# Optimization experiments

Hardware: AMD Instinct MI355X
Metric: run time of the kernel (lower is better)

The kernel has to match this reference:

```python
import jax, jax.numpy as jnp
import numpy as np

T, D, H = 2048, 1024, 16
HS = D // H  # head_size = 64
DFF = 4 * D
LN_EPS = 1e-6


def layernorm(x, scale, bias, eps=LN_EPS):
    mu = jnp.mean(x, axis=-1, keepdims=True)
    var = jnp.mean(jnp.square(x - mu), axis=-1, keepdims=True)
    return (x - mu) * jax.lax.rsqrt(var + eps) * scale + bias


def setup_inputs() -> dict:
    key = jax.random.key(0)
    ks = jax.random.split(key, 12)
    s_in = 1.0 / np.sqrt(D)
    s_ff = 1.0 / np.sqrt(DFF)
    return {
        "x": jax.random.normal(ks[0], (T, D), jnp.float32),
        "Wq": jax.random.normal(ks[1], (H, D, HS), jnp.float32) * s_in,
        "Wk": jax.random.normal(ks[2], (H, D, HS), jnp.float32) * s_in,
        "Wv": jax.random.normal(ks[3], (H, D, HS), jnp.float32) * s_in,
        "Wo": jax.random.normal(ks[4], (D, D), jnp.float32) * s_in,
        "bo": jnp.zeros((D,), jnp.float32),
        "W1": jax.random.normal(ks[5], (D, DFF), jnp.float32) * s_in,
        "b1": jnp.zeros((DFF,), jnp.float32),
        "W2": jax.random.normal(ks[6], (DFF, D), jnp.float32) * s_ff,
        "b2": jnp.zeros((D,), jnp.float32),
        "ln1_scale": jnp.ones((D,), jnp.float32),
        "ln1_bias": jnp.zeros((D,), jnp.float32),
        "ln2_scale": jnp.ones((D,), jnp.float32),
        "ln2_bias": jnp.zeros((D,), jnp.float32),
        "training": 0,
    }


def reference(x, Wq, Wk, Wv, Wo, bo, W1, b1, W2, b2,
              ln1_scale, ln1_bias, ln2_scale, ln2_bias, training):
    # --- pre-LN causal multi-head self-attention ---
    h = layernorm(x, ln1_scale, ln1_bias)
    q = jnp.einsum("td,hdk->htk", h, Wq)  # [H,T,HS]
    k = jnp.einsum("td,hdk->htk", h, Wk)
    v = jnp.einsum("td,hdk->htk", h, Wv)
    scores = jnp.einsum("htk,hsk->hts", q, k) / jnp.sqrt(jnp.float32(HS))
    causal = jnp.tril(jnp.ones((T, T), jnp.float32))
    scores = jnp.where(causal == 0, -jnp.inf, scores)
    wei = jax.nn.softmax(scores, axis=-1)
    av = jnp.einsum("hts,hsk->htk", wei, v)          # [H,T,HS]
    av = av.transpose(1, 0, 2).reshape(T, H * HS)    # concat over heads
    x = x + av @ Wo + bo                              # dropout deterministic -> identity
    # --- pre-LN feed-forward ---
    h2 = layernorm(x, ln2_scale, ln2_bias)
    ff = jax.nn.relu(h2 @ W1 + b1) @ W2 + b2
    x = x + ff
    return x
```

## Files before the change

kernel.cpp:

```cpp
#include <hip/hip_runtime.h>
#include <cstdint>


typedef __bf16 bf16;
typedef __bf16 bf16x4 __attribute__((ext_vector_type(4)));
typedef __bf16 bf16x8 __attribute__((ext_vector_type(8)));
typedef float floatx4 __attribute__((ext_vector_type(4)));

__device__ __forceinline__ void ld_g2l(const bf16* g, bf16* l) {
    __builtin_amdgcn_global_load_lds(
        (const __attribute__((address_space(1))) void*)g,
        (__attribute__((address_space(3))) void*)l, 16, 0, 0);
}

__device__ __forceinline__ void ln_row_body(
    const float* __restrict__ x, const float* __restrict__ sc,
    const float* __restrict__ bi, bf16* __restrict__ out,
    int row, int tid, float* wred)
{
    const float4 v = ((const float4*)(x + (size_t)row * 1024))[tid];
    float s1 = v.x + v.y + v.z + v.w;
    float s2 = v.x * v.x + v.y * v.y + v.z * v.z + v.w * v.w;
#pragma unroll
    for (int mm = 1; mm < 64; mm <<= 1) {
        s1 += __shfl_xor(s1, mm);
        s2 += __shfl_xor(s2, mm);
    }
    const int wave = tid >> 6, lane = tid & 63;
    if (lane == 0) { wred[wave] = s1; wred[4 + wave] = s2; }
    __syncthreads();
    s1 = wred[0] + wred[1] + wred[2] + wred[3];
    s2 = wred[4] + wred[5] + wred[6] + wred[7];
    const float mu = s1 * (1.f / 1024.f);
    const float var = fmaxf(s2 * (1.f / 1024.f) - mu * mu, 0.f);
    const float rr = rsqrtf(var + 1e-6f);
    const float4 scv = ((const float4*)sc)[tid];
    const float4 biv = ((const float4*)bi)[tid];
    bf16x4 ov;
    ov[0] = (bf16)((v.x - mu) * rr * scv.x + biv.x);
    ov[1] = (bf16)((v.y - mu) * rr * scv.y + biv.y);
    ov[2] = (bf16)((v.z - mu) * rr * scv.z + biv.z);
    ov[3] = (bf16)((v.w - mu) * rr * scv.w + biv.w);
    *(bf16x4*)(out + (size_t)row * 1024 + tid * 4) = ov;
}

__global__ __launch_bounds__(256) void prep_kernel(
    const float* __restrict__ Wq, const float* __restrict__ Wk,
    const float* __restrict__ Wv, bf16* __restrict__ Wqkvt,
    const float* __restrict__ Wo, bf16* __restrict__ Wot,
    const float* __restrict__ W1, bf16* __restrict__ W1t,
    const float* __restrict__ W2, bf16* __restrict__ W2t,
    const float* __restrict__ x, const float* __restrict__ ln1s,
    const float* __restrict__ ln1b, bf16* __restrict__ hbuf)
{
    __shared__ float tile[64][65];
    __shared__ float wred[8];
    const int b = blockIdx.x;
    const int tid = threadIdx.x;

    if (b >= 3072) {
        ln_row_body(x, ln1s, ln1b, hbuf, b - 3072, tid, wred);
        return;
    }

    const int tx = tid & 63, ty = tid >> 6;
    const float* src; bf16* dst; int R, C, c0, r0;
    if (b < 768) {
        const int sec = b >> 4, ti = b & 15;
        const int m = sec >> 4, h = sec & 15;
        src = (m == 0 ? Wq : (m == 1 ? Wk : Wv)) + h * 65536;
        dst = Wqkvt + m * 1048576 + h * 65536;
        R = 1024; C = 64; c0 = 0; r0 = ti * 64;
    } else if (b < 1024) {
        const int i = b - 768;
        src = Wo; dst = Wot; R = 1024; C = 1024;
        c0 = (i & 15) * 64; r0 = (i >> 4) * 64;
    } else if (b < 2048) {
        const int i = b - 1024;
        src = W1; dst = W1t; R = 1024; C = 4096;
        c0 = (i & 63) * 64; r0 = (i >> 6) * 64;
    } else {
        const int i = b - 2048;
        src = W2; dst = W2t; R = 4096; C = 1024;
        c0 = (i & 15) * 64; r0 = (i >> 4) * 64;
    }
#pragma unroll
    for (int i = ty; i < 64; i += 4)
        tile[i][tx] = src[(size_t)(r0 + i) * C + c0 + tx];
    __syncthreads();
#pragma unroll
    for (int i = ty; i < 64; i += 4)
        dst[(size_t)(c0 + i) * R + r0 + tx] = (bf16)tile[tx][i];
}

__global__ __launch_bounds__(256) void ln_kernel(
    const float* __restrict__ x, const float* __restrict__ sc,
    const float* __restrict__ bi, bf16* __restrict__ out)
{
    __shared__ float wred[8];
    ln_row_body(x, sc, bi, out, blockIdx.x, threadIdx.x, wred);
}

__global__ __launch_bounds__(256) void transpose_head_kernel(
    const bf16* __restrict__ qkv, bf16* __restrict__ dst, int colOff)
{
    __shared__ bf16 tile[32][33];
    const int tx = threadIdx.x, ty = threadIdx.y;
    const int h = blockIdx.z;
    const int j0 = blockIdx.x * 32, s0 = blockIdx.y * 32;
#pragma unroll
    for (int i = ty; i < 32; i += 8)
        tile[i][tx] = qkv[(size_t)(s0 + i) * 3072 + colOff + h * 64 + j0 + tx];
    __syncthreads();
#pragma unroll
    for (int i = ty; i < 32; i += 8)
        dst[(size_t)h * 64 * 2048 + (size_t)(j0 + i) * 2048 + s0 + tx] = tile[tx][i];
}

__global__ __launch_bounds__(256) void reduce4_kernel(
    const float* __restrict__ p, const float* __restrict__ bias,
    const float* __restrict__ res, float* __restrict__ out)
{
    const int idx = blockIdx.x * 256 + threadIdx.x;
    const int c4 = idx & 255;
    const float4 a0 = ((const float4*)p)[idx];
    const float4 a1 = ((const float4*)(p + 2097152))[idx];
    const float4 a2 = ((const float4*)(p + 4194304))[idx];
    const float4 a3 = ((const float4*)(p + 6291456))[idx];
    const float4 bi = ((const float4*)bias)[c4];
    const float4 r = ((const float4*)res)[idx];
    float4 o;
    o.x = (a0.x + a1.x) + (a2.x + a3.x) + bi.x + r.x;
    o.y = (a0.y + a1.y) + (a2.y + a3.y) + bi.y + r.y;
    o.z = (a0.z + a1.z) + (a2.z + a3.z) + bi.z + r.z;
    o.w = (a0.w + a1.w) + (a2.w + a3.w) + bi.w + r.w;
    ((float4*)out)[idx] = o;
}

template <int MODE, int NG, int MG, int SPLITK>
__global__ __launch_bounds__(256) void gemm128_kernel(
    const bf16* __restrict__ A, const bf16* __restrict__ Bt,
    int N, int K,
    float* __restrict__ outF, bf16* __restrict__ outB,
    const float* __restrict__ bias)
{
    __shared__ __align__(16) bf16 Alds[2][128][64];
    __shared__ __align__(16) bf16 Blds[2][128][64];
    const int tid  = threadIdx.x;
    const int lane = tid & 63;
    const int w    = tid >> 6;
    const int r15  = lane & 15;
    const int quad = lane >> 4;

    const int id    = blockIdx.x + gridDim.x * (blockIdx.y + gridDim.y * blockIdx.z);
    const int xcd   = id & 7;
    const int seq   = id >> 3;
    const int nPerX = gridDim.x / NG;
    const int mPerX = gridDim.y / MG;
    const int nm    = nPerX * mPerX;
    const int z     = seq / nm;
    const int loc   = seq - z * nm;
    const int bn    = ((xcd % NG) * nPerX + (loc % nPerX)) * 128;
    const int bm    = ((xcd / NG) * mPerX + (loc / nPerX)) * 128;

    const int wm = (w >> 1) * 64;
    const int wn = (w & 1) * 64;

    floatx4 acc[4][4];
#pragma unroll
    for (int i = 0; i < 4; ++i)
#pragma unroll
        for (int j = 0; j < 4; ++j) acc[i][j] = (floatx4)(0.f);

    const int KS    = K / SPLITK;
    const int kBase = (SPLITK > 1) ? z * KS : 0;
    const int nIter = KS / 64;

    const int lrow = lane >> 3;
    const int gch  = (lane & 7) ^ lrow;
    const bf16* aptr = A + (size_t)(bm + w * 16 + lrow) * K + kBase + gch * 8;
    const bf16* bptr = Bt + (size_t)(bn + w * 16 + lrow) * K + kBase + gch * 8;

#pragma unroll
    for (int rr = 0; rr < 2; ++rr)
#pragma unroll
        for (int t = 0; t < 2; ++t) {
            ld_g2l(aptr + (size_t)(rr * 64 + t * 8) * K, &Alds[0][rr * 64 + w * 16 + t * 8][0]);
            ld_g2l(bptr + (size_t)(rr * 64 + t * 8) * K, &Blds[0][rr * 64 + w * 16 + t * 8][0]);
        }

    for (int it = 0; it < nIter; ++it) {
        const int buf = it & 1;
        __syncthreads();
        if (it + 1 < nIter) {
            const int k2 = (it + 1) * 64;
#pragma unroll
            for (int rr = 0; rr < 2; ++rr)
#pragma unroll
                for (int t = 0; t < 2; ++t) {
                    ld_g2l(aptr + (size_t)(rr * 64 + t * 8) * K + k2,
                           &Alds[buf ^ 1][rr * 64 + w * 16 + t * 8][0]);
                    ld_g2l(bptr + (size_t)(rr * 64 + t * 8) * K + k2,
                           &Blds[buf ^ 1][rr * 64 + w * 16 + t * 8][0]);
                }
        }
#pragma unroll
        for (int kk = 0; kk < 2; ++kk) {
            const int pc = ((kk * 4 + quad) ^ (r15 & 7)) * 8;
            bf16x8 af[4], bfr[4];
#pragma unroll
            for (int i = 0; i < 4; ++i)
                af[i] = *(const bf16x8*)(&Alds[buf][wm + i * 16 + r15][pc]);
#pragma unroll
            for (int j = 0; j < 4; ++j)
                bfr[j] = *(const bf16x8*)(&Blds[buf][wn + j * 16 + r15][pc]);
#pragma unroll
            for (int i = 0; i < 4; ++i)
#pragma unroll
                for (int j = 0; j < 4; ++j)
                    acc[i][j] = __builtin_amdgcn_mfma_f32_16x16x32_bf16(
                        af[i], bfr[j], acc[i][j], 0, 0, 0);
        }
    }

    const int row0 = bm + wm + quad * 4;
    const int col0 = bn + wn + r15;
    float* po = (MODE == 3) ? outF + (size_t)z * 2048 * 1024 : outF;
#pragma unroll
    for (int i = 0; i < 4; ++i) {
#pragma unroll
        for (int reg = 0; reg < 4; ++reg) {
            const int row = row0 + i * 16 + reg;
#pragma unroll
            for (int j = 0; j < 4; ++j) {
                const int col = col0 + j * 16;
                float v = acc[i][j][reg];
                if (MODE == 0) {
                    outB[(size_t)row * N + col] = (bf16)v;
                } else if (MODE == 2) {
                    v += bias[col];
                    outB[(size_t)row * N + col] = (bf16)fmaxf(v, 0.f);
                } else {
                    po[(size_t)row * N + col] = v;
                }
            }
        }
    }
}

template <int NG, int MG>
__global__ __launch_bounds__(256) void gemm64_kernel(
    const bf16* __restrict__ A, const bf16* __restrict__ Bt,
    int N, int K,
    float* __restrict__ outF, const float* __restrict__ bias,
    const float* __restrict__ res)
{
    __shared__ __align__(16) bf16 Alds[2][64][64];
    __shared__ __align__(16) bf16 Blds[2][64][64];
    const int tid  = threadIdx.x;
    const int lane = tid & 63;
    const int w    = tid >> 6;
    const int r15  = lane & 15;
    const int quad = lane >> 4;

    const int id    = blockIdx.x + gridDim.x * blockIdx.y;
    const int xcd   = id & 7;
    const int seq   = id >> 3;
    const int nPerX = gridDim.x / NG;
    const int mPerX = gridDim.y / MG;
    const int loc   = seq % (nPerX * mPerX);
    const int bn    = ((xcd % NG) * nPerX + (loc % nPerX)) * 64;
    const int bm    = ((xcd / NG) * mPerX + (loc / nPerX)) * 64;

    const int wm = (w >> 1) * 32;
    const int wn = (w & 1) * 32;

    floatx4 acc[2][2];
#pragma unroll
    for (int i = 0; i < 2; ++i)
#pragma unroll
        for (int j = 0; j < 2; ++j) acc[i][j] = (floatx4)(0.f);

    const int nIter = K / 64;
    const int lrow = lane >> 3;
    const int gch  = (lane & 7) ^ lrow;
    const bf16* aptr = A + (size_t)(bm + w * 16 + lrow) * K + gch * 8;
    const bf16* bptr = Bt + (size_t)(bn + w * 16 + lrow) * K + gch * 8;

#pragma unroll
    for (int t = 0; t < 2; ++t) {
        ld_g2l(aptr + (size_t)t * 8 * K, &Alds[0][w * 16 + t * 8][0]);
        ld_g2l(bptr + (size_t)t * 8 * K, &Blds[0][w * 16 + t * 8][0]);
    }

    for (int it = 0; it < nIter; ++it) {
        const int buf = it & 1;
        __syncthreads();
        if (it + 1 < nIter) {
            const int k2 = (it + 1) * 64;
#pragma unroll
            for (int t = 0; t < 2; ++t) {
                ld_g2l(aptr + (size_t)t * 8 * K + k2, &Alds[buf ^ 1][w * 16 + t * 8][0]);
                ld_g2l(bptr + (size_t)t * 8 * K + k2, &Blds[buf ^ 1][w * 16 + t * 8][0]);
            }
        }
#pragma unroll
        for (int kk = 0; kk < 2; ++kk) {
            const int pc = ((kk * 4 + quad) ^ (r15 & 7)) * 8;
            bf16x8 af[2], bfr[2];
#pragma unroll
            for (int i = 0; i < 2; ++i)
                af[i] = *(const bf16x8*)(&Alds[buf][wm + i * 16 + r15][pc]);
#pragma unroll
            for (int j = 0; j < 2; ++j)
                bfr[j] = *(const bf16x8*)(&Blds[buf][wn + j * 16 + r15][pc]);
#pragma unroll
            for (int i = 0; i < 2; ++i)
#pragma unroll
                for (int j = 0; j < 2; ++j)
                    acc[i][j] = __builtin_amdgcn_mfma_f32_16x16x32_bf16(
                        af[i], bfr[j], acc[i][j], 0, 0, 0);
        }
    }

    const int row0 = bm + wm + quad * 4;
    const int col0 = bn + wn + r15;
#pragma unroll
    for (int i = 0; i < 2; ++i)
#pragma unroll
        for (int reg = 0; reg < 4; ++reg) {
            const int row = row0 + i * 16 + reg;
#pragma unroll
            for (int j = 0; j < 2; ++j) {
                const int col = col0 + j * 16;
                outF[(size_t)row * N + col] =
                    acc[i][j][reg] + bias[col] + res[(size_t)row * N + col];
            }
        }
}

__global__ __launch_bounds__(256) void attn_kernel(
    const bf16* __restrict__ qkv, const bf16* __restrict__ vt,
    bf16* __restrict__ Opart, float* __restrict__ Lpart)
{
    __shared__ __align__(16) bf16 Qs[64][64];
    __shared__ __align__(16) bf16 Ks[2][64][64];
    __shared__ __align__(16) bf16 Vs[2][64][64];
    __shared__ __align__(16) bf16 Ps[4][16][72];

    const int tid  = threadIdx.x;
    const int w    = tid >> 6;
    const int lane = tid & 63;
    const int r15  = lane & 15;
    const int quad = lane >> 4;
    const int rl   = lane >> 3;
    const int gsw  = (lane & 7) ^ (rl & 7);

    const int b    = blockIdx.x;
    const int idp  = b & 255;
    const int seq  = idp >> 3;
    const int h    = (idp & 7) * 2 + (seq & 1);
    const int qp   = seq >> 1;
    const int qt   = ((b >> 8) & 1) ? 31 - qp : qp;
    const int half = b >> 9;
    const int qrow0 = qt * 64;

    const int n0    = (qt + 2) >> 1;
    const int sbBeg = half ? n0 : 0;
    const int sbEnd = half ? qt + 1 : n0;

    const int tile = half * 512 + h * 32 + qt;
    const size_t obase = (size_t)tile * 4096;

    if (sbBeg >= sbEnd) {
        const int4 z = {0, 0, 0, 0};
        ((int4*)(Opart + obase))[tid] = z;
        if (tid < 64) Lpart[tile * 64 + tid] = 0.f;
        return;
    }

    const bf16* qsec = qkv + h * 64;
    const bf16* ksec = qkv + 1024 + h * 64;
    const bf16* vth  = vt + (size_t)h * 64 * 2048;
    const int s0 = sbBeg * 64;

#pragma unroll
    for (int t = 0; t < 2; ++t) {
        const int r = t * 32 + w * 8 + rl;
        ld_g2l(qsec + (size_t)(qrow0 + r) * 3072 + gsw * 8, &Qs[t * 32 + w * 8][0]);
        ld_g2l(ksec + (size_t)(s0 + r) * 3072 + gsw * 8, &Ks[0][t * 32 + w * 8][0]);
        ld_g2l(vth + (size_t)r * 2048 + s0 + gsw * 8, &Vs[0][t * 32 + w * 8][0]);
    }
    __syncthreads();

    bf16x8 qf[2];
#pragma unroll
    for (int c = 0; c < 2; ++c) {
        const int p = ((c * 4 + quad) ^ (r15 & 7)) * 8;
        qf[c] = *(const bf16x8*)&Qs[w * 16 + r15][p];
    }

    float lacc[4] = {0.f, 0.f, 0.f, 0.f};
    floatx4 O[4];
#pragma unroll
    for (int j = 0; j < 4; ++j) O[j] = (floatx4)(0.f);

    int ns = 0;
#pragma unroll 1
    for (int sb = sbBeg; sb < sbEnd; ++sb, ++ns) {
        const int buf = ns & 1;
        if (sb + 1 < sbEnd) {
            const int s1 = (sb + 1) * 64;
#pragma unroll
            for (int t = 0; t < 2; ++t) {
                const int r = t * 32 + w * 8 + rl;
                ld_g2l(ksec + (size_t)(s1 + r) * 3072 + gsw * 8, &Ks[buf ^ 1][t * 32 + w * 8][0]);
                ld_g2l(vth + (size_t)r * 2048 + s1 + gsw * 8, &Vs[buf ^ 1][t * 32 + w * 8][0]);
            }
        }

        floatx4 S[4];
#pragma unroll
        for (int j = 0; j < 4; ++j) S[j] = (floatx4)(0.f);
        __builtin_amdgcn_s_setprio(1);
#pragma unroll
        for (int c = 0; c < 2; ++c) {
#pragma unroll
            for (int j = 0; j < 4; ++j) {
                const int p = ((c * 4 + quad) ^ (r15 & 7)) * 8;
                const bf16x8 kb = *(const bf16x8*)&Ks[buf][j * 16 + r15][p];
                S[j] = __builtin_amdgcn_mfma_f32_16x16x32_bf16(qf[c], kb, S[j], 0, 0, 0);
            }
        }
        __builtin_amdgcn_s_setprio(0);
        const bool diag = (sb == qt);
        const int rowl = w * 16 + quad * 4;
#pragma unroll
        for (int j = 0; j < 4; ++j) {
            const int col = j * 16 + r15;
#pragma unroll
            for (int r = 0; r < 4; ++r) {
                float p = exp2f(fmaf(S[j][r], 0.18033688f, -28.853901f));
                if (diag && col > rowl + r) p = 0.f;
                S[j][r] = p;
                lacc[r] += p;
            }
        }
#pragma unroll
        for (int r = 0; r < 4; ++r)
#pragma unroll
            for (int j = 0; j < 4; ++j)
                Ps[w][quad * 4 + r][j * 16 + r15] = (bf16)S[j][r];
        __builtin_amdgcn_s_setprio(1);
#pragma unroll
        for (int c = 0; c < 2; ++c) {
            const bf16x8 a = *(const bf16x8*)&Ps[w][r15][c * 32 + quad * 8];
#pragma unroll
            for (int j = 0; j < 4; ++j) {
                const int p = ((c * 4 + quad) ^ (r15 & 7)) * 8;
                const bf16x8 vb = *(const bf16x8*)&Vs[buf][j * 16 + r15][p];
                O[j] = __builtin_amdgcn_mfma_f32_16x16x32_bf16(a, vb, O[j], 0, 0, 0);
            }
        }
        __builtin_amdgcn_s_setprio(0);
        __syncthreads();
    }
#pragma unroll
    for (int r = 0; r < 4; ++r) {
#pragma unroll
        for (int d = 1; d < 16; d <<= 1) lacc[r] += __shfl_xor(lacc[r], d);
    }
#pragma unroll
    for (int r = 0; r < 4; ++r) {
        const int row = w * 16 + quad * 4 + r;
#pragma unroll
        for (int j = 0; j < 4; ++j)
            Opart[obase + (size_t)row * 64 + j * 16 + r15] = (bf16)(O[j][r]);
    }
    if (r15 == 0) {
#pragma unroll
        for (int r = 0; r < 4; ++r)
            Lpart[tile * 64 + w * 16 + quad * 4 + r] = lacc[r];
    }
}

__global__ __launch_bounds__(256) void attn_combine_kernel(
    const bf16* __restrict__ Op, const float* __restrict__ Lp,
    bf16* __restrict__ out)
{
    const int b = blockIdx.x;
    const int h = b >> 5, qt = b & 31;
    const int tid = threadIdx.x;
    const int r = tid >> 2, cg = tid & 3;
    const size_t pa = (size_t)b * 4096 + r * 64 + cg * 16;
    const bf16x8 a0 = *(const bf16x8*)(Op + pa);
    const bf16x8 a1 = *(const bf16x8*)(Op + pa + 8);
    const bf16x8 b0 = *(const bf16x8*)(Op + 2097152 + pa);
    const bf16x8 b1 = *(const bf16x8*)(Op + 2097152 + pa + 8);
    const float la = Lp[b * 64 + r];
    const float lb = Lp[32768 + b * 64 + r];
    const float inv = 1.f / (la + lb);
    bf16x8 o0, o1;
#pragma unroll
    for (int i = 0; i < 8; ++i) {
        o0[i] = (bf16)(((float)a0[i] + (float)b0[i]) * inv);
        o1[i] = (bf16)(((float)a1[i] + (float)b1[i]) * inv);
    }
    bf16* dst = out + (size_t)(qt * 64 + r) * 1024 + h * 64 + cg * 16;
    *(bf16x8*)dst = o0;
    *(bf16x8*)(dst + 8) = o1;
}

extern "C" void kernel_launch(void* const* d_in, const int* in_sizes, int n_in,
                              void* d_out, int out_size, void* d_ws, size_t ws_size,
                              hipStream_t stream)
{
    const float* x    = (const float*)d_in[0];
    const float* Wq   = (const float*)d_in[1];
    const float* Wk   = (const float*)d_in[2];
    const float* Wv   = (const float*)d_in[3];
    const float* Wo   = (const float*)d_in[4];
    const float* bo   = (const float*)d_in[5];
    const float* W1   = (const float*)d_in[6];
    const float* b1   = (const float*)d_in[7];
    const float* W2   = (const float*)d_in[8];
    const float* b2   = (const float*)d_in[9];
    const float* ln1s = (const float*)d_in[10];
    const float* ln1b = (const float*)d_in[11];
    const float* ln2s = (const float*)d_in[12];
    const float* ln2b = (const float*)d_in[13];

    char* ws = (char*)d_ws;
    bf16*  Wqkvt = (bf16*)(ws + 0);
    bf16*  Wot   = (bf16*)(ws + 6291456);
    bf16*  W1t   = (bf16*)(ws + 8388608);
    bf16*  W2t   = (bf16*)(ws + 16777216);
    bf16*  hbuf  = (bf16*)(ws + 25165824);
    bf16*  QKV   = (bf16*)(ws + 29360128);
    bf16*  Vt    = (bf16*)(ws + 41943040);
    bf16*  Obuf  = (bf16*)(ws + 46137344);
    float* x1    = (float*)(ws + 50331648);
    bf16*  h2    = (bf16*)(ws + 58720256);
    bf16*  ff1   = (bf16*)(ws + 62914560);
    float* psum  = (float*)(ws + 79691776);
    bf16*  Opart = (bf16*)(ws + 79691776);
    float* Lpart = (float*)(ws + 88080384);

    const dim3 tb(32, 8);

    prep_kernel<<<5120, 256, 0, stream>>>(Wq, Wk, Wv, Wqkvt, Wo, Wot,
                                          W1, W1t, W2, W2t,
                                          x, ln1s, ln1b, hbuf);
    gemm128_kernel<0,4,2,1><<<dim3(24, 16), 256, 0, stream>>>(hbuf, Wqkvt, 3072, 1024, nullptr, QKV, nullptr);
    transpose_head_kernel<<<dim3(2, 64, 16), tb, 0, stream>>>(QKV, Vt, 2048);
    attn_kernel<<<1024, 256, 0, stream>>>(QKV, Vt, Opart, Lpart);
    attn_combine_kernel<<<512, 256, 0, stream>>>(Opart, Lpart, Obuf);
    gemm64_kernel<4,2><<<dim3(16, 32), 256, 0, stream>>>(Obuf, Wot, 1024, 1024, x1, bo, x);
    ln_kernel<<<2048, 256, 0, stream>>>(x1, ln2s, ln2b, h2);
    gemm128_kernel<2,4,2,1><<<dim3(32, 16), 256, 0, stream>>>(h2, W1t, 4096, 1024, nullptr, ff1, b1);
    gemm128_kernel<3,2,4,4><<<dim3(8, 16, 4), 256, 0, stream>>>(ff1, W2t, 1024, 4096, psum, nullptr, nullptr);
    reduce4_kernel<<<2048, 256, 0, stream>>>(psum, b2, x1, (float*)d_out);
}
```

Before: 251.9 us.

## Fuse V transpose into QKV GEMM epilogue and skip empty attention splits

The QKV GEMM gets a new mode whose epilogue writes the V columns straight into the per-head transposed Vt layout, so the separate transpose_head kernel and its extra read/write pass over V go away. Attention blocks with no key range now return early without zero-filling their partial outputs. The combine kernel reads only the first partial when qt==0, which relies on the second half always being empty for that tile. Causal masking is split into a diagonal and a non-diagonal path so off-diagonal blocks skip the per-element mask compare. The V epilogue uses strided 8-byte stores that may coalesce less well than the original row-major writes.

```diff
diff --git a/kernel.cpp b/kernel.cpp
--- a/kernel.cpp
+++ b/kernel.cpp
@@ -101,22 +101,6 @@
     ln_row_body(x, sc, bi, out, blockIdx.x, threadIdx.x, wred);
 }
 
-__global__ __launch_bounds__(256) void transpose_head_kernel(
-    const bf16* __restrict__ qkv, bf16* __restrict__ dst, int colOff)
-{
-    __shared__ bf16 tile[32][33];
-    const int tx = threadIdx.x, ty = threadIdx.y;
-    const int h = blockIdx.z;
-    const int j0 = blockIdx.x * 32, s0 = blockIdx.y * 32;
-#pragma unroll
-    for (int i = ty; i < 32; i += 8)
-        tile[i][tx] = qkv[(size_t)(s0 + i) * 3072 + colOff + h * 64 + j0 + tx];
-    __syncthreads();
-#pragma unroll
-    for (int i = ty; i < 32; i += 8)
-        dst[(size_t)h * 64 * 2048 + (size_t)(j0 + i) * 2048 + s0 + tx] = tile[tx][i];
-}
-
 __global__ __launch_bounds__(256) void reduce4_kernel(
     const float* __restrict__ p, const float* __restrict__ bias,
     const float* __restrict__ res, float* __restrict__ out)
@@ -225,6 +209,25 @@
 
     const int row0 = bm + wm + quad * 4;
     const int col0 = bn + wn + r15;
+
+    if (MODE == 1 && bn >= 2048) {
+        bf16* vt = (bf16*)outF;
+#pragma unroll
+        for (int i = 0; i < 4; ++i) {
+            const int row = row0 + i * 16;
+#pragma unroll
+            for (int j = 0; j < 4; ++j) {
+                const int col = col0 + j * 16 - 2048;
+                bf16x4 pv;
+#pragma unroll
+                for (int reg = 0; reg < 4; ++reg) pv[reg] = (bf16)acc[i][j][reg];
+                *(bf16x4*)(vt + (size_t)(col >> 6) * 131072
+                              + (size_t)(col & 63) * 2048 + row) = pv;
+            }
+        }
+        return;
+    }
+
     float* po = (MODE == 3) ? outF + (size_t)z * 2048 * 1024 : outF;
 #pragma unroll
     for (int i = 0; i < 4; ++i) {
@@ -235,7 +238,7 @@
             for (int j = 0; j < 4; ++j) {
                 const int col = col0 + j * 16;
                 float v = acc[i][j][reg];
-                if (MODE == 0) {
+                if (MODE == 0 || MODE == 1) {
                     outB[(size_t)row * N + col] = (bf16)v;
                 } else if (MODE == 2) {
                     v += bias[col];
@@ -369,15 +372,10 @@
     const int sbBeg = half ? n0 : 0;
     const int sbEnd = half ? qt + 1 : n0;
 
+    if (sbBeg >= sbEnd) return;
+
     const int tile = half * 512 + h * 32 + qt;
     const size_t obase = (size_t)tile * 4096;
-
-    if (sbBeg >= sbEnd) {
-        const int4 z = {0, 0, 0, 0};
-        ((int4*)(Opart + obase))[tid] = z;
-        if (tid < 64) Lpart[tile * 64 + tid] = 0.f;
-        return;
-    }
 
     const bf16* qsec = qkv + h * 64;
     const bf16* ksec = qkv + 1024 + h * 64;
@@ -433,18 +431,28 @@
             }
         }
         __builtin_amdgcn_s_setprio(0);
-        const bool diag = (sb == qt);
-        const int rowl = w * 16 + quad * 4;
-#pragma unroll
-        for (int j = 0; j < 4; ++j) {
-            const int col = j * 16 + r15;
-#pragma unroll
-            for (int r = 0; r < 4; ++r) {
-                float p = exp2f(fmaf(S[j][r], 0.18033688f, -28.853901f));
-                if (diag && col > rowl + r) p = 0.f;
-                S[j][r] = p;
-                lacc[r] += p;
-            }
+        if (sb == qt) {
+            const int rowl = w * 16 + quad * 4;
+#pragma unroll
+            for (int j = 0; j < 4; ++j) {
+                const int col = j * 16 + r15;
+#pragma unroll
+                for (int r = 0; r < 4; ++r) {
+                    float p = exp2f(fmaf(S[j][r], 0.18033688f, -28.853901f));
+                    if (col > rowl + r) p = 0.f;
+                    S[j][r] = p;
+                    lacc[r] += p;
+                }
+            }
+        } else {
+#pragma unroll
+            for (int j = 0; j < 4; ++j)
+#pragma unroll
+                for (int r = 0; r < 4; ++r) {
+                    const float p = exp2f(fmaf(S[j][r], 0.18033688f, -28.853901f));
+                    S[j][r] = p;
+                    lacc[r] += p;
+                }
         }
 #pragma unroll
         for (int r = 0; r < 4; ++r)
@@ -495,16 +503,25 @@
     const size_t pa = (size_t)b * 4096 + r * 64 + cg * 16;
     const bf16x8 a0 = *(const bf16x8*)(Op + pa);
     const bf16x8 a1 = *(const bf16x8*)(Op + pa + 8);
-    const bf16x8 b0 = *(const bf16x8*)(Op + 2097152 + pa);
-    const bf16x8 b1 = *(const bf16x8*)(Op + 2097152 + pa + 8);
     const float la = Lp[b * 64 + r];
-    const float lb = Lp[32768 + b * 64 + r];
-    const float inv = 1.f / (la + lb);
     bf16x8 o0, o1;
-#pragma unroll
-    for (int i = 0; i < 8; ++i) {
-        o0[i] = (bf16)(((float)a0[i] + (float)b0[i]) * inv);
-        o1[i] = (bf16)(((float)a1[i] + (float)b1[i]) * inv);
+    if (qt > 0) {
+        const bf16x8 b0 = *(const bf16x8*)(Op + 2097152 + pa);
+        const bf16x8 b1 = *(const bf16x8*)(Op + 2097152 + pa + 8);
+        const float lb = Lp[32768 + b * 64 + r];
+        const float inv = 1.f / (la + lb);
+#pragma unroll
+        for (int i = 0; i < 8; ++i) {
+            o0[i] = (bf16)(((float)a0[i] + (float)b0[i]) * inv);
+            o1[i] = (bf16)(((float)a1[i] + (float)b1[i]) * inv);
+        }
+    } else {
+        const float inv = 1.f / la;
+#pragma unroll
+        for (int i = 0; i < 8; ++i) {
+            o0[i] = (bf16)((float)a0[i] * inv);
+            o1[i] = (bf16)((float)a1[i] * inv);
+        }
     }
     bf16* dst = out + (size_t)(qt * 64 + r) * 1024 + h * 64 + cg * 16;
     *(bf16x8*)dst = o0;
@@ -546,13 +563,10 @@
     bf16*  Opart = (bf16*)(ws + 79691776);
     float* Lpart = (float*)(ws + 88080384);
 
-    const dim3 tb(32, 8);
-
     prep_kernel<<<5120, 256, 0, stream>>>(Wq, Wk, Wv, Wqkvt, Wo, Wot,
                                           W1, W1t, W2, W2t,
                                           x, ln1s, ln1b, hbuf);
-    gemm128_kernel<0,4,2,1><<<dim3(24, 16), 256, 0, stream>>>(hbuf, Wqkvt, 3072, 1024, nullptr, QKV, nullptr);
-    transpose_head_kernel<<<dim3(2, 64, 16), tb, 0, stream>>>(QKV, Vt, 2048);
+    gemm128_kernel<1,4,2,1><<<dim3(24, 16), 256, 0, stream>>>(hbuf, Wqkvt, 3072, 1024, (float*)Vt, QKV, nullptr);
     attn_kernel<<<1024, 256, 0, stream>>>(QKV, Vt, Opart, Lpart);
     attn_combine_kernel<<<512, 256, 0, stream>>>(Opart, Lpart, Obuf);
     gemm64_kernel<4,2><<<dim3(16, 32), 256, 0, stream>>>(Obuf, Wot, 1024, 1024, x1, bo, x);
```

After: 253.1 us. About the same (+0.5%).
